# Optimization experiments

Measured on AMD Instinct MI355X. Metric: run time of the kernel, lower is better.

The kernel has to match this reference:

```python
import jax, jax.numpy as jnp
import numpy as np

NUM_EXPERTS = 8
NUM_SPIKE_EXPERTS = 2
TOTAL_EXPERTS = NUM_EXPERTS + NUM_SPIKE_EXPERTS
D_IN = 512
HIDDEN = 1024  # expert_dim == spike_expert_capacity
D_OUT = 256
TOP_K = 2


def setup_inputs() -> dict:
    key = jax.random.key(0)
    ks = jax.random.split(key, 8)
    B, T = 32768, 16
    x = jax.random.normal(ks[0], (B, D_IN), dtype=jnp.float32)
    spike_indicators = jax.random.uniform(ks[1], (B, T), dtype=jnp.float32)
    s = 0.02
    Wr = jax.random.normal(ks[2], (D_IN, TOTAL_EXPERTS), dtype=jnp.float32) * s
    br = jnp.zeros((TOTAL_EXPERTS,), dtype=jnp.float32)
    W1 = jax.random.normal(ks[3], (TOTAL_EXPERTS, D_IN, HIDDEN), dtype=jnp.float32) * s
    b1 = jnp.zeros((TOTAL_EXPERTS, HIDDEN), dtype=jnp.float32)
    W2 = jax.random.normal(ks[4], (TOTAL_EXPERTS, HIDDEN, D_OUT), dtype=jnp.float32) * s
    b2 = jnp.zeros((TOTAL_EXPERTS, D_OUT), dtype=jnp.float32)
    return {"x": x, "spike_indicators": spike_indicators, "Wr": Wr, "br": br,
            "W1": W1, "b1": b1, "W2": W2, "b2": b2}


def reference(x, spike_indicators, Wr, br, W1, b1, W2, b2):
    # Router logits (plain Dense router branch)
    router_logits = x @ Wr + br                                   # [B, E]
    # Spike-expert routing bias: mean spike indicator added to spike experts only
    spike_mask = jnp.concatenate(
        [jnp.zeros((NUM_EXPERTS,), x.dtype), jnp.ones((NUM_SPIKE_EXPERTS,), x.dtype)])
    avg_spike = jnp.mean(spike_indicators, axis=1, keepdims=True)  # [B, 1]
    adjusted = router_logits + avg_spike * spike_mask[None, :]
    router_probs = jax.nn.softmax(adjusted, axis=-1)               # [B, E]
    top_k_probs, top_k_idx = jax.lax.top_k(router_probs, TOP_K)    # [B, K]
    top_k_norm = top_k_probs / (jnp.sum(top_k_probs, axis=1, keepdims=True) + 1e-9)
    # All experts computed for all tokens (matches original dense loop)
    h = jax.nn.relu(jnp.einsum('bd,edh->beh', x, W1) + b1[None])   # [B, E, H]
    expert_stack = jnp.einsum('beh,eho->beo', h, W2) + b2[None]    # [B, E, O]
    # Gather top-k expert outputs per token and combine
    gathered = jnp.take_along_axis(expert_stack, top_k_idx[:, :, None], axis=1)  # [B, K, O]
    mixed = jnp.sum(gathered * top_k_norm[:, :, None], axis=1)     # [B, O]
    return mixed
```

## Files before the change

kernel.cpp:

```cpp
#include <hip/hip_runtime.h>
#include <hip/hip_bf16.h>
#include <stdint.h>
#include <stddef.h>

typedef __attribute__((ext_vector_type(8))) short short8;
typedef __attribute__((ext_vector_type(4))) float f32x4;

#define NTOK 32768
#define DIN 512
#define HID 1024
#define DOUT 256
#define NEXP 10

#define TW1_BLOCKS 1280
#define TW2_BLOCKS 640
#define RT_BLOCKS  512

__device__ __forceinline__ unsigned short f2bf(float f) {
  unsigned int u = __float_as_uint(f);
  u += 0x7fffu + ((u >> 16) & 1u);
  return (unsigned short)(u >> 16);
}

__device__ __forceinline__ unsigned long long pack4bf(float4 v) {
  return (unsigned long long)f2bf(v.x) | ((unsigned long long)f2bf(v.y) << 16) |
         ((unsigned long long)f2bf(v.z) << 32) | ((unsigned long long)f2bf(v.w) << 48);
}

__device__ __forceinline__ void gld16(void* lds, const void* g) {
  __builtin_amdgcn_global_load_lds(
      (const __attribute__((address_space(1))) unsigned int*)g,
      (__attribute__((address_space(3))) unsigned int*)lds, 16, 0, 0);
}

union PrepSmem {
  unsigned short tile[64][72];
  struct {
    int i0[64]; int i1[64]; float w0[64]; float w1[64];
    int hist[NEXP]; int base_[NEXP]; int loc[NEXP];
  } rt;
};

__global__ __launch_bounds__(256) void k_prep(
    const float* __restrict__ x, const float* __restrict__ spike,
    const float* __restrict__ Wr, const float* __restrict__ br,
    const float* __restrict__ W1, const float* __restrict__ W2,
    unsigned short* __restrict__ xb, unsigned short* __restrict__ w1t,
    unsigned short* __restrict__ w2t, int* __restrict__ cnt,
    int* __restrict__ tok, float* __restrict__ wgt, float* __restrict__ out) {
  __shared__ PrepSmem sm;
  int bid = blockIdx.x;
  int tid = threadIdx.x;

  if (bid < TW1_BLOCKS + TW2_BLOCKS) {
    const float* in; unsigned short* outp; int R, C, bx, by, bz;
    if (bid < TW1_BLOCKS) {
      int r = bid; bz = r >> 7; r &= 127; by = r >> 4; bx = r & 15;
      in = W1; outp = w1t; R = DIN; C = HID;
    } else {
      int r = bid - TW1_BLOCKS; bz = r >> 6; r &= 63; by = r >> 2; bx = r & 3;
      in = W2; outp = w2t; R = HID; C = DOUT;
    }
    const float* ip = in + ((size_t)bz * R + by * 64) * C + bx * 64;
    int rr = tid >> 2, c0 = (tid & 3) * 16;
    const float* p = ip + (size_t)rr * C + c0;
#pragma unroll
    for (int j = 0; j < 16; j += 4) {
      float4 v = *(const float4*)(p + j);
      sm.tile[rr][c0 + j + 0] = f2bf(v.x);
      sm.tile[rr][c0 + j + 1] = f2bf(v.y);
      sm.tile[rr][c0 + j + 2] = f2bf(v.z);
      sm.tile[rr][c0 + j + 3] = f2bf(v.w);
    }
    __syncthreads();
    unsigned short* op = outp + ((size_t)bz * C + bx * 64) * R + by * 64;
    int c = tid >> 2, r0 = (tid & 3) * 16;
    unsigned short* q = op + (size_t)c * R + r0;
    union { short8 v; unsigned short u[8]; } t0, t1;
#pragma unroll
    for (int j = 0; j < 8; j++) { t0.u[j] = sm.tile[r0 + j][c]; t1.u[j] = sm.tile[r0 + 8 + j][c]; }
    *(short8*)(q) = t0.v;
    *(short8*)(q + 8) = t1.v;
    return;
  }

  int rb = bid - (TW1_BLOCKS + TW2_BLOCKS);
  int wave = tid >> 6, lane = tid & 63;
  {
    float4 z = {0.f, 0.f, 0.f, 0.f};
    float4* ob = (float4*)(out + (size_t)rb * 64 * DOUT);
#pragma unroll
    for (int i = 0; i < 16; i++) ob[i * 256 + tid] = z;
  }
  if (tid < NEXP) { sm.rt.hist[tid] = 0; sm.rt.loc[tid] = 0; }
  __syncthreads();
  float4 wv[NEXP][2];
  float brr[NEXP];
#pragma unroll
  for (int e = 0; e < NEXP; e++) {
    brr[e] = br[e];
#pragma unroll
    for (int h = 0; h < 2; h++) {
      int d0 = h * 256 + lane * 4;
      wv[e][h] = (float4){Wr[(size_t)(d0 + 0) * NEXP + e], Wr[(size_t)(d0 + 1) * NEXP + e],
                          Wr[(size_t)(d0 + 2) * NEXP + e], Wr[(size_t)(d0 + 3) * NEXP + e]};
    }
  }
  for (int t = 0; t < 16; t++) {
    int slot = wave * 16 + t;
    int b = rb * 64 + slot;
    const float4* xr4 = (const float4*)(x + (size_t)b * DIN);
    float4 xv0 = xr4[lane], xv1 = xr4[64 + lane];
    *(unsigned long long*)(xb + (size_t)b * DIN + lane * 4) = pack4bf(xv0);
    *(unsigned long long*)(xb + (size_t)b * DIN + 256 + lane * 4) = pack4bf(xv1);
    float lg[NEXP];
#pragma unroll
    for (int e = 0; e < NEXP; e++) {
      lg[e] = xv0.x * wv[e][0].x + xv0.y * wv[e][0].y + xv0.z * wv[e][0].z + xv0.w * wv[e][0].w +
              xv1.x * wv[e][1].x + xv1.y * wv[e][1].y + xv1.z * wv[e][1].z + xv1.w * wv[e][1].w;
    }
#pragma unroll
    for (int off = 32; off > 0; off >>= 1) {
#pragma unroll
      for (int e = 0; e < NEXP; e++) lg[e] += __shfl_xor(lg[e], off);
    }
    float sv = spike[(size_t)b * 16 + (lane & 15)];
    sv += __shfl_xor(sv, 8); sv += __shfl_xor(sv, 4);
    sv += __shfl_xor(sv, 2); sv += __shfl_xor(sv, 1);
    float avg = sv * 0.0625f;
#pragma unroll
    for (int e = 0; e < NEXP; e++) lg[e] += brr[e];
    lg[8] += avg; lg[9] += avg;
    float mx = lg[0];
#pragma unroll
    for (int e = 1; e < NEXP; e++) mx = fmaxf(mx, lg[e]);
    float p[NEXP], ps = 0.f;
#pragma unroll
    for (int e = 0; e < NEXP; e++) { p[e] = __expf(lg[e] - mx); ps += p[e]; }
    int i0 = 0; float p0 = p[0];
#pragma unroll
    for (int e = 1; e < NEXP; e++) if (p[e] > p0) { p0 = p[e]; i0 = e; }
    float p1 = -1.f; int i1 = 0;
#pragma unroll
    for (int e = 0; e < NEXP; e++) if (e != i0 && p[e] > p1) { p1 = p[e]; i1 = e; }
    float inv = 1.f / (p0 + p1 + ps * 1e-9f);
    if (lane == 0) {
      sm.rt.i0[slot] = i0; sm.rt.i1[slot] = i1;
      sm.rt.w0[slot] = p0 * inv; sm.rt.w1[slot] = p1 * inv;
      atomicAdd(&sm.rt.hist[i0], 1); atomicAdd(&sm.rt.hist[i1], 1);
    }
  }
  __syncthreads();
  if (tid < NEXP) sm.rt.base_[tid] = atomicAdd(&cnt[tid], sm.rt.hist[tid]);
  __syncthreads();
  if (tid < 64) {
    int b = rb * 64 + tid;
    int i0 = sm.rt.i0[tid], i1 = sm.rt.i1[tid];
    int s0 = sm.rt.base_[i0] + atomicAdd(&sm.rt.loc[i0], 1);
    tok[i0 * NTOK + s0] = b; wgt[i0 * NTOK + s0] = sm.rt.w0[tid];
    int s1 = sm.rt.base_[i1] + atomicAdd(&sm.rt.loc[i1], 1);
    tok[i1 * NTOK + s1] = b; wgt[i1 * NTOK + s1] = sm.rt.w1[tid];
  }
}

__global__ __launch_bounds__(256, 2) void k_moe(
    const unsigned short* __restrict__ xb, const unsigned short* __restrict__ w1t,
    const unsigned short* __restrict__ w2t, const float* __restrict__ b1,
    const float* __restrict__ b2, const int* __restrict__ cnt,
    const int* __restrict__ tok, const float* __restrict__ wgt,
    float* __restrict__ out) {
  int e = blockIdx.y;
  int n = cnt[e];
  int tile = blockIdx.x;
  if (tile * 64 >= n) return;
  __shared__ unsigned short xa[2][4096];
  __shared__ unsigned short wp[2][8192];
  __shared__ unsigned short hs[8192];
  __shared__ int stok[64];
  __shared__ float swgt[64];
  int tid = threadIdx.x;
  if (tid < 64) {
    int idx = tile * 64 + tid;
    bool v = idx < n;
    stok[tid] = v ? tok[e * NTOK + idx] : 0;
    swgt[tid] = v ? wgt[e * NTOK + idx] : 0.f;
  }
  __syncthreads();
  int wave = tid >> 6, lane = tid & 63, quad = lane >> 4, l16 = lane & 15;
  int wm = wave & 1, wn = wave >> 1;
  int srow = tid >> 3;
  int c8 = (tid & 7) ^ (srow & 7);
  const unsigned short* gx0 = xb + (size_t)stok[srow] * DIN + c8 * 8;
  const unsigned short* gx1 = xb + (size_t)stok[32 + srow] * DIN + c8 * 8;
  const unsigned short* w1e = w1t + (size_t)e * HID * DIN;
  const unsigned short* w2e = w2t + (size_t)e * DOUT * HID;
  const unsigned short* gb1 = w1e + (size_t)srow * DIN + c8 * 8;
  const unsigned short* gb2 = w2e + (size_t)(2 * srow + (c8 >> 2)) * HID + (c8 & 3) * 8;
  int ra0 = wm * 32 + l16, ra1 = ra0 + 16;
  int rh0 = wn * 64 + l16;
  int ro0 = wn * 128 + l16;
  f32x4 acc2[2][8];
#pragma unroll
  for (int nt = 0; nt < 8; nt++) {
    float bv = b2[e * DOUT + wn * 128 + nt * 16 + l16];
    acc2[0][nt] = (f32x4){bv, bv, bv, bv};
    acc2[1][nt] = (f32x4){bv, bv, bv, bv};
  }
  gld16(xa[0] + (size_t)tid * 8, gx0);
  gld16(xa[0] + ((size_t)tid + 256) * 8, gx1);
#pragma unroll
  for (int s = 0; s < 4; s++)
    gld16(wp[0] + ((size_t)s * 256 + tid) * 8, gb1 + (size_t)s * 32 * DIN);

  for (int hc = 0; hc < 8; hc++) {
    f32x4 acc1[2][4];
#pragma unroll
    for (int nt = 0; nt < 4; nt++) {
      float bv = b1[e * HID + hc * 128 + wn * 64 + nt * 16 + l16];
      acc1[0][nt] = (f32x4){bv, bv, bv, bv};
      acc1[1][nt] = (f32x4){bv, bv, bv, bv};
    }
#pragma unroll 1
    for (int ks = 0; ks < 8; ks++) {
      __syncthreads();
      if (ks < 7) {
        gld16(xa[(ks + 1) & 1] + (size_t)tid * 8, gx0 + (ks + 1) * 64);
        gld16(xa[(ks + 1) & 1] + ((size_t)tid + 256) * 8, gx1 + (ks + 1) * 64);
#pragma unroll
        for (int s = 0; s < 4; s++)
          gld16(wp[(ks + 1) & 1] + ((size_t)s * 256 + tid) * 8,
                gb1 + (size_t)hc * 128 * DIN + (size_t)s * 32 * DIN + (ks + 1) * 64);
      } else {
#pragma unroll
        for (int s = 0; s < 4; s++)
          gld16(wp[0] + ((size_t)s * 256 + tid) * 8,
                gb2 + (size_t)s * 64 * HID + hc * 128);
      }
      const unsigned short* xab = xa[ks & 1];
      const unsigned short* w1b = wp[ks & 1];
#pragma unroll
      for (int ki2 = 0; ki2 < 2; ki2++) {
        int cq = ki2 * 4 + quad;
        short8 af[2], bf[4];
        af[0] = *(const short8*)(xab + (ra0 * 8 + (cq ^ (ra0 & 7))) * 8);
        af[1] = *(const short8*)(xab + (ra1 * 8 + (cq ^ (ra1 & 7))) * 8);
#pragma unroll
        for (int nt = 0; nt < 4; nt++) {
          int r = rh0 + nt * 16;
          bf[nt] = *(const short8*)(w1b + (r * 8 + (cq ^ (r & 7))) * 8);
        }
#pragma unroll
        for (int mt = 0; mt < 2; mt++)
#pragma unroll
          for (int nt = 0; nt < 4; nt++)
            acc1[mt][nt] = __builtin_amdgcn_mfma_f32_16x16x32_bf16(
                af[mt], bf[nt], acc1[mt][nt], 0, 0, 0);
      }
    }
#pragma unroll
    for (int mt = 0; mt < 2; mt++) {
#pragma unroll
      for (int nt = 0; nt < 4; nt++) {
        int col = wn * 64 + nt * 16 + l16;
        int c16 = col >> 3, co = col & 7;
#pragma unroll
        for (int r4 = 0; r4 < 4; r4++) {
          int r = wm * 32 + mt * 16 + quad * 4 + r4;
          float v = acc1[mt][nt][r4];
          hs[(r * 16 + (c16 ^ (r & 15))) * 8 + co] = f2bf(v > 0.f ? v : 0.f);
        }
      }
    }
#pragma unroll 1
    for (int k2 = 0; k2 < 4; k2++) {
      __syncthreads();
      if (k2 < 3) {
#pragma unroll
        for (int s = 0; s < 4; s++)
          gld16(wp[(k2 + 1) & 1] + ((size_t)s * 256 + tid) * 8,
                gb2 + (size_t)s * 64 * HID + hc * 128 + (k2 + 1) * 32);
      } else if (hc < 7) {
        gld16(xa[0] + (size_t)tid * 8, gx0);
        gld16(xa[0] + ((size_t)tid + 256) * 8, gx1);
#pragma unroll
        for (int s = 0; s < 4; s++)
          gld16(wp[0] + ((size_t)s * 256 + tid) * 8,
                gb1 + (size_t)(hc + 1) * 128 * DIN + (size_t)s * 32 * DIN);
      }
      const unsigned short* b2b = wp[k2 & 1];
      int c16 = k2 * 4 + quad;
      short8 af[2], bf[8];
      af[0] = *(const short8*)(hs + (ra0 * 16 + (c16 ^ (ra0 & 15))) * 8);
      af[1] = *(const short8*)(hs + (ra1 * 16 + (c16 ^ (ra1 & 15))) * 8);
#pragma unroll
      for (int nt = 0; nt < 8; nt++) {
        int rr = ro0 + nt * 16;
        int inner = (((rr & 1) << 2) | quad) ^ ((rr >> 1) & 7);
        bf[nt] = *(const short8*)(b2b + ((rr >> 1) * 8 + inner) * 8);
      }
#pragma unroll
      for (int mt = 0; mt < 2; mt++)
#pragma unroll
        for (int nt = 0; nt < 8; nt++)
          acc2[mt][nt] = __builtin_amdgcn_mfma_f32_16x16x32_bf16(
              af[mt], bf[nt], acc2[mt][nt], 0, 0, 0);
    }
  }
#pragma unroll
  for (int mt = 0; mt < 2; mt++) {
#pragma unroll
    for (int r4 = 0; r4 < 4; r4++) {
      int m = wm * 32 + mt * 16 + quad * 4 + r4;
      float wv = swgt[m];
      if (wv != 0.f) {
        int t = stok[m];
        float* op = out + (size_t)t * DOUT + wn * 128 + l16;
#pragma unroll
        for (int nt = 0; nt < 8; nt++)
          atomicAdd(op + nt * 16, acc2[mt][nt][r4] * wv);
      }
    }
  }
}

extern "C" void kernel_launch(void* const* d_in, const int* in_sizes, int n_in,
                              void* d_out, int out_size, void* d_ws, size_t ws_size,
                              hipStream_t stream) {
  (void)in_sizes; (void)n_in; (void)ws_size; (void)out_size;
  const float* x     = (const float*)d_in[0];
  const float* spike = (const float*)d_in[1];
  const float* Wr    = (const float*)d_in[2];
  const float* br    = (const float*)d_in[3];
  const float* W1    = (const float*)d_in[4];
  const float* b1    = (const float*)d_in[5];
  const float* W2    = (const float*)d_in[6];
  const float* b2    = (const float*)d_in[7];
  float* out = (float*)d_out;
  char* ws = (char*)d_ws;
  unsigned short* xb  = (unsigned short*)(ws + 0);
  unsigned short* w1t = (unsigned short*)(ws + 33554432);
  unsigned short* w2t = (unsigned short*)(ws + 44040192);
  int*   cnt          = (int*)(ws + 49303552);
  int*   tok          = (int*)(ws + 49303616);
  float* wgt          = (float*)(ws + 50614336);

  hipMemsetAsync(cnt, 0, 64, stream);
  k_prep<<<TW1_BLOCKS + TW2_BLOCKS + RT_BLOCKS, 256, 0, stream>>>(
      x, spike, Wr, br, W1, W2, xb, w1t, w2t, cnt, tok, wgt, out);
  k_moe<<<dim3(512, NEXP), 256, 0, stream>>>(xb, w1t, w2t, b1, b2, cnt, tok, wgt, out);
}
```

Before: 426.5 us.

## Drop LDS double buffering to raise occupancy in fused MoE kernel

Replaces the double-buffered LDS staging of x and weight tiles with single buffers, and drops the prefetch of the next tile so each step loads, syncs, then computes. Token index and weight staging in shared memory are removed; they are now read directly from global memory. Launch bounds go from 2 to 4 blocks per SM, aiming to hide latency through more resident waves instead of software pipelining. The cost is an extra barrier per k-step and loss of load/compute overlap within a block, plus register pressure from the tighter bound possibly causing spills.

```diff
diff --git a/kernel.cpp b/kernel.cpp
--- a/kernel.cpp
+++ b/kernel.cpp
@@ -163,7 +163,7 @@
   }
 }
 
-__global__ __launch_bounds__(256, 2) void k_moe(
+__global__ __launch_bounds__(256, 4) void k_moe(
     const unsigned short* __restrict__ xb, const unsigned short* __restrict__ w1t,
     const unsigned short* __restrict__ w2t, const float* __restrict__ b1,
     const float* __restrict__ b2, const int* __restrict__ cnt,
@@ -173,25 +173,19 @@
   int n = cnt[e];
   int tile = blockIdx.x;
   if (tile * 64 >= n) return;
-  __shared__ unsigned short xa[2][4096];
-  __shared__ unsigned short wp[2][8192];
+  __shared__ unsigned short xa[4096];
+  __shared__ unsigned short wp[8192];
   __shared__ unsigned short hs[8192];
-  __shared__ int stok[64];
-  __shared__ float swgt[64];
   int tid = threadIdx.x;
-  if (tid < 64) {
-    int idx = tile * 64 + tid;
-    bool v = idx < n;
-    stok[tid] = v ? tok[e * NTOK + idx] : 0;
-    swgt[tid] = v ? wgt[e * NTOK + idx] : 0.f;
-  }
-  __syncthreads();
   int wave = tid >> 6, lane = tid & 63, quad = lane >> 4, l16 = lane & 15;
   int wm = wave & 1, wn = wave >> 1;
   int srow = tid >> 3;
   int c8 = (tid & 7) ^ (srow & 7);
-  const unsigned short* gx0 = xb + (size_t)stok[srow] * DIN + c8 * 8;
-  const unsigned short* gx1 = xb + (size_t)stok[32 + srow] * DIN + c8 * 8;
+  int i0 = tile * 64 + srow, i1 = i0 + 32;
+  int t0 = i0 < n ? tok[e * NTOK + i0] : 0;
+  int t1 = i1 < n ? tok[e * NTOK + i1] : 0;
+  const unsigned short* gx0 = xb + (size_t)t0 * DIN + c8 * 8;
+  const unsigned short* gx1 = xb + (size_t)t1 * DIN + c8 * 8;
   const unsigned short* w1e = w1t + (size_t)e * HID * DIN;
   const unsigned short* w2e = w2t + (size_t)e * DOUT * HID;
   const unsigned short* gb1 = w1e + (size_t)srow * DIN + c8 * 8;
@@ -206,12 +200,6 @@
     acc2[0][nt] = (f32x4){bv, bv, bv, bv};
     acc2[1][nt] = (f32x4){bv, bv, bv, bv};
   }
-  gld16(xa[0] + (size_t)tid * 8, gx0);
-  gld16(xa[0] + ((size_t)tid + 256) * 8, gx1);
-#pragma unroll
-  for (int s = 0; s < 4; s++)
-    gld16(wp[0] + ((size_t)s * 256 + tid) * 8, gb1 + (size_t)s * 32 * DIN);
-
   for (int hc = 0; hc < 8; hc++) {
     f32x4 acc1[2][4];
 #pragma unroll
@@ -220,34 +208,25 @@
       acc1[0][nt] = (f32x4){bv, bv, bv, bv};
       acc1[1][nt] = (f32x4){bv, bv, bv, bv};
     }
-#pragma unroll 1
     for (int ks = 0; ks < 8; ks++) {
       __syncthreads();
-      if (ks < 7) {
-        gld16(xa[(ks + 1) & 1] + (size_t)tid * 8, gx0 + (ks + 1) * 64);
-        gld16(xa[(ks + 1) & 1] + ((size_t)tid + 256) * 8, gx1 + (ks + 1) * 64);
-#pragma unroll
-        for (int s = 0; s < 4; s++)
-          gld16(wp[(ks + 1) & 1] + ((size_t)s * 256 + tid) * 8,
-                gb1 + (size_t)hc * 128 * DIN + (size_t)s * 32 * DIN + (ks + 1) * 64);
-      } else {
-#pragma unroll
-        for (int s = 0; s < 4; s++)
-          gld16(wp[0] + ((size_t)s * 256 + tid) * 8,
-                gb2 + (size_t)s * 64 * HID + hc * 128);
-      }
-      const unsigned short* xab = xa[ks & 1];
-      const unsigned short* w1b = wp[ks & 1];
+      gld16(xa + (size_t)tid * 8, gx0 + ks * 64);
+      gld16(xa + ((size_t)tid + 256) * 8, gx1 + ks * 64);
+#pragma unroll
+      for (int s = 0; s < 4; s++)
+        gld16(wp + ((size_t)s * 256 + tid) * 8,
+              gb1 + (size_t)hc * 128 * DIN + (size_t)s * 32 * DIN + ks * 64);
+      __syncthreads();
 #pragma unroll
       for (int ki2 = 0; ki2 < 2; ki2++) {
         int cq = ki2 * 4 + quad;
         short8 af[2], bf[4];
-        af[0] = *(const short8*)(xab + (ra0 * 8 + (cq ^ (ra0 & 7))) * 8);
-        af[1] = *(const short8*)(xab + (ra1 * 8 + (cq ^ (ra1 & 7))) * 8);
+        af[0] = *(const short8*)(xa + (ra0 * 8 + (cq ^ (ra0 & 7))) * 8);
+        af[1] = *(const short8*)(xa + (ra1 * 8 + (cq ^ (ra1 & 7))) * 8);
 #pragma unroll
         for (int nt = 0; nt < 4; nt++) {
           int r = rh0 + nt * 16;
-          bf[nt] = *(const short8*)(w1b + (r * 8 + (cq ^ (r & 7))) * 8);
+          bf[nt] = *(const short8*)(wp + (r * 8 + (cq ^ (r & 7))) * 8);
         }
 #pragma unroll
         for (int mt = 0; mt < 2; mt++)
@@ -271,23 +250,13 @@
         }
       }
     }
-#pragma unroll 1
     for (int k2 = 0; k2 < 4; k2++) {
       __syncthreads();
-      if (k2 < 3) {
-#pragma unroll
-        for (int s = 0; s < 4; s++)
-          gld16(wp[(k2 + 1) & 1] + ((size_t)s * 256 + tid) * 8,
-                gb2 + (size_t)s * 64 * HID + hc * 128 + (k2 + 1) * 32);
-      } else if (hc < 7) {
-        gld16(xa[0] + (size_t)tid * 8, gx0);
-        gld16(xa[0] + ((size_t)tid + 256) * 8, gx1);
-#pragma unroll
-        for (int s = 0; s < 4; s++)
-          gld16(wp[0] + ((size_t)s * 256 + tid) * 8,
-                gb1 + (size_t)(hc + 1) * 128 * DIN + (size_t)s * 32 * DIN);
-      }
-      const unsigned short* b2b = wp[k2 & 1];
+#pragma unroll
+      for (int s = 0; s < 4; s++)
+        gld16(wp + ((size_t)s * 256 + tid) * 8,
+              gb2 + (size_t)s * 64 * HID + hc * 128 + k2 * 32);
+      __syncthreads();
       int c16 = k2 * 4 + quad;
       short8 af[2], bf[8];
       af[0] = *(const short8*)(hs + (ra0 * 16 + (c16 ^ (ra0 & 15))) * 8);
@@ -296,7 +265,7 @@
       for (int nt = 0; nt < 8; nt++) {
         int rr = ro0 + nt * 16;
         int inner = (((rr & 1) << 2) | quad) ^ ((rr >> 1) & 7);
-        bf[nt] = *(const short8*)(b2b + ((rr >> 1) * 8 + inner) * 8);
+        bf[nt] = *(const short8*)(wp + ((rr >> 1) * 8 + inner) * 8);
       }
 #pragma unroll
       for (int mt = 0; mt < 2; mt++)
@@ -311,9 +280,10 @@
 #pragma unroll
     for (int r4 = 0; r4 < 4; r4++) {
       int m = wm * 32 + mt * 16 + quad * 4 + r4;
-      float wv = swgt[m];
-      if (wv != 0.f) {
-        int t = stok[m];
+      int idx = tile * 64 + m;
+      if (idx < n) {
+        float wv = wgt[e * NTOK + idx];
+        int t = tok[e * NTOK + idx];
         float* op = out + (size_t)t * DOUT + wn * 128 + l16;
 #pragma unroll
         for (int nt = 0; nt < 8; nt++)
```

Result: slower. 545.1 us (+27.8%).
